# Kernel tuning notes

Hardware: AMD Instinct MI355X
Metric: run time of the kernel (lower is better)

Reference implementation:

```python
import jax, jax.numpy as jnp
import numpy as np

B, C, N, K, H = 8, 64, 4096, 32, 4
D = C // H  # head dim = 16
EPS = 1e-5  # BatchNorm eps (torch default)


def setup_inputs() -> dict:
    key = jax.random.key(0)
    ks = jax.random.split(key, 7)
    s = 0.05
    return {
        "x": jax.random.normal(ks[0], (B, C, N), jnp.float32),
        "wq": jax.random.normal(ks[1], (C, C), jnp.float32) * s,
        "wk": jax.random.normal(ks[2], (C, C), jnp.float32) * s,
        "wv": jax.random.normal(ks[3], (C, C), jnp.float32) * s,
        "w1": jax.random.normal(ks[4], (4 * C, C), jnp.float32) * s,
        "w2": jax.random.normal(ks[5], (C, 4 * C), jnp.float32) * s,
        "g1": jnp.ones((C,), jnp.float32),
        "b1": jnp.zeros((C,), jnp.float32),
        "g2": jnp.ones((C,), jnp.float32),
        "b2": jnp.zeros((C,), jnp.float32),
    }


def _bn(f, g, b):
    # BatchNorm1d in training mode: stats over (batch, points) per channel.
    # f: (B, N, C)
    mu = jnp.mean(f, axis=(0, 1))
    var = jnp.var(f, axis=(0, 1))  # biased, as torch uses for normalization
    return (f - mu) * jax.lax.rsqrt(var + EPS) * g + b


def reference(x, wq, wk, wv, w1, w2, g1, b1, g2, b2):
    feat = jnp.transpose(x, (0, 2, 1))  # (B, N, C)
    # KNN in feature space: negative squared distances, take top-K largest
    sq = jnp.sum(feat * feat, axis=-1)  # (B, N)
    neg_d = 2.0 * jnp.einsum('bnc,bmc->bnm', feat, feat) - sq[:, :, None] - sq[:, None, :]
    _, idx = jax.lax.top_k(neg_d, K)  # (B, N, K) int32
    # gather neighbors and form diffs
    nbrs = jax.vmap(lambda p, i: p[i])(feat, idx)  # (B, N, K, C)
    diff = nbrs - feat[:, :, None, :]
    # 1x1-conv projections (bias-free linear over channels)
    q = jnp.einsum('bnc,oc->bno', feat, wq).reshape(B, N, H, D)
    k = jnp.einsum('bnkc,oc->bnko', diff, wk).reshape(B, N, K, H, D)
    v = jnp.einsum('bnkc,oc->bnko', diff, wv).reshape(B, N, K, H, D)
    energy = jnp.einsum('bnhd,bnkhd->bnhk', q, k) / jnp.sqrt(jnp.float32(D))
    attn = jax.nn.softmax(energy, axis=-1)  # softmax over K neighbors
    out = jnp.einsum('bnhk,bnkhd->bnhd', attn, v).reshape(B, N, C)  # H-major merge
    f1 = _bn(feat + out, g1, b1)
    hid = jnp.einsum('bnc,oc->bno', f1, w1)
    hid = jnp.where(hid > 0, hid, 0.2 * hid)  # LeakyReLU(0.2)
    ff = jnp.einsum('bno,co->bnc', hid, w2)
    f2 = _bn(f1 + ff, g2, b2)
    return jnp.transpose(f2, (0, 2, 1))  # (B, C, N)
```

## Files before the change

### kernel.cpp

```cpp
#include <hip/hip_runtime.h>

#define Bdim 8
#define Cdim 64
#define Ndim 4096
#define Kdim 32
#define ROWS (Bdim*Ndim)
#define BN_EPS 1e-5f

using f32x4  = __attribute__((ext_vector_type(4))) float;
using f16x8  = __attribute__((ext_vector_type(8))) _Float16;

__device__ __forceinline__ float dot4(float4 a, float4 b){
  return a.x*b.x + a.y*b.y + a.z*b.z + a.w*b.w;
}
__device__ __forceinline__ int wofs(int o, int g){ return o*64 + (((g ^ ((o>>2)&7)))<<2); }
__device__ __forceinline__ unsigned keyOf(float f){
  unsigned u = __float_as_uint(f);
  return (u & 0x80000000u) ? ~u : (u ^ 0x80000000u);
}

__global__ __launch_bounds__(256) void prep_proj_kernel(const float* __restrict__ x,
    const float* __restrict__ wq, const float* __restrict__ wk,
    const float* __restrict__ wv,
    float* __restrict__ sq,
    float* __restrict__ Qo, float* __restrict__ PKo, float* __restrict__ PVo,
    float* __restrict__ accZ,
    float* __restrict__ featT, unsigned short* __restrict__ xh)
{
  __shared__ __align__(16) float ftile[64*68];
  __shared__ __align__(16) float Ws[3][64*64];
  const int tid = threadIdx.x;
  const int blk = blockIdx.x;
  const int b  = blk & 7;
  const int n0 = (blk >> 3) * 64;
  const size_t rowBase = (size_t)b*Ndim + n0;
  if (blk == 0) accZ[tid] = 0.f;
  for (int k=0;k<16;++k){
    int idx = tid + (k<<8);
    int c = idx>>6, nn = idx&63;
    ftile[nn*68+c] = x[((size_t)b*64+c)*Ndim + n0 + nn];
  }
  {
    const float* wp[3] = {wq, wk, wv};
    for (int m=0;m<3;++m)
      for (int k=0;k<16;++k){
        int idx = tid + (k<<8);
        int o = idx>>6, c = idx&63;
        Ws[m][wofs(o, c>>2) + (c&3)] = wp[m][o*64 + c];
      }
  }
  __syncthreads();
  for (int k=0;k<16;++k){
    int idx = tid + (k<<8);
    int r = idx>>6, c = idx&63;
    float v = ftile[r*68+c];
    size_t o = (rowBase + r)*64 + c;
    featT[o] = v;
    _Float16 hh = (_Float16)v;
    xh[o] = *reinterpret_cast<unsigned short*>(&hh);
  }
  if (tid < 64){
    float a = 0.f;
    #pragma unroll
    for (int c=0;c<64;++c){ float v = ftile[tid*68+c]; a += v*v; }
    sq[b*Ndim + n0 + tid] = a;
  }
  const int tr = tid>>4, to = tid&15;
  float* outp[3] = {Qo, PKo, PVo};
  for (int m=0;m<3;++m){
    float acc[4][4];
    #pragma unroll
    for (int r=0;r<4;++r){ acc[r][0]=0.f; acc[r][1]=0.f; acc[r][2]=0.f; acc[r][3]=0.f; }
    #pragma unroll 4
    for (int c4=0;c4<16;++c4){
      float4 f[4], w[4];
      #pragma unroll
      for (int r=0;r<4;++r)  f[r] = *(const float4*)&ftile[(4*tr+r)*68 + (c4<<2)];
      #pragma unroll
      for (int oo=0;oo<4;++oo) w[oo] = *(const float4*)&Ws[m][wofs(4*to+oo, c4)];
      #pragma unroll
      for (int r=0;r<4;++r)
        #pragma unroll
        for (int oo=0;oo<4;++oo)
          acc[r][oo] += dot4(f[r], w[oo]);
    }
    #pragma unroll
    for (int r=0;r<4;++r){
      float4 v; v.x=acc[r][0]; v.y=acc[r][1]; v.z=acc[r][2]; v.w=acc[r][3];
      *(float4*)&outp[m][(rowBase + 4*tr + r)*64 + 4*to] = v;
    }
  }
}

__global__ __launch_bounds__(1024) void knn_attn_kernel(
    const float* __restrict__ sq,
    const float* __restrict__ Qm, const float* __restrict__ PKm, const float* __restrict__ PVm,
    const float* __restrict__ featT, const unsigned short* __restrict__ xh,
    float* __restrict__ t1, float* __restrict__ bn1s, float* __restrict__ bn1q)
{
  __shared__ __align__(16) unsigned char smem[43200];
  float* fnS  = (float*)smem;
  float* qvS  = (float*)(smem + 4096);
  float* pknS = (float*)(smem + 8192);
  float* pvnS = (float*)(smem + 12288);
  unsigned short* dbuf = (unsigned short*)(smem + 16384);
  int*   candI  = (int*)(smem + 16384);
  float* red1   = (float*)(smem + 20480);
  float* red2   = (float*)(smem + 24576);
  float* enS    = (float*)(smem + 32896);
  int*   outIdx = (int*)(smem + 41088);
  float* sqnS   = (float*)(smem + 43136);

  const int tid  = threadIdx.x;
  const int lane = tid & 63;
  const int w    = tid >> 6;
  const int blk  = blockIdx.x;
  const int b    = blk & 7;
  const int n0   = (blk >> 3) << 4;
  const size_t b4096 = (size_t)b << 12;

  {
    int j = tid>>6, c = tid&63;
    size_t ro = (b4096 + n0 + j)*64 + c;
    fnS[tid]  = featT[ro];
    qvS[tid]  = Qm[ro];
    pknS[tid] = PKm[ro];
    pvnS[tid] = PVm[ro];
    if (tid < 16) sqnS[tid] = sq[b4096 + n0 + tid];
    if (tid < 512) outIdx[tid] = n0 + (tid>>5);
  }
  __syncthreads();

  const unsigned short* xhb = xh + (b4096 << 6);
  const float* sqb = sq + b4096;
  const int l15  = lane & 15;
  const int acol = (lane >> 4) << 3;
  const int qrow = (lane >> 4) << 2;

  unsigned kk[32];

  {
    f16x8 a0 = *(const f16x8*)&xhb[(size_t)(n0 + l15)*64 + acol];
    f16x8 a1 = *(const f16x8*)&xhb[(size_t)(n0 + l15)*64 + acol + 32];
    #pragma unroll
    for (int ch=0; ch<16; ++ch){
      unsigned short* bw = dbuf + (ch&1)*(16*258);
      const int brow = (ch<<8) + (w<<4) + l15;
      f16x8 b0 = *(const f16x8*)&xhb[(size_t)brow*64 + acol];
      f16x8 b1 = *(const f16x8*)&xhb[(size_t)brow*64 + acol + 32];
      f32x4 acc = {0.f,0.f,0.f,0.f};
      acc = __builtin_amdgcn_mfma_f32_16x16x32_f16(a0, b0, acc, 0, 0, 0);
      acc = __builtin_amdgcn_mfma_f32_16x16x32_f16(a1, b1, acc, 0, 0, 0);
      float sm = sqb[brow];
      #pragma unroll
      for (int r=0;r<4;++r){
        float v = fmaf(2.f, acc[r], -sm);
        int k16 = (int)fmaf(v, 128.f, 40960.f);
        k16 = k16 < 0 ? 0 : (k16 > 65535 ? 65535 : k16);
        bw[(qrow+r)*258 + (w<<4) + l15] = (unsigned short)k16;
      }
      __syncthreads();
      unsigned k01 = *(const unsigned*)&bw[w*258 + (lane<<2)];
      unsigned k23 = *(const unsigned*)&bw[w*258 + (lane<<2) + 2];
      kk[(ch<<1)]   = k01;
      kk[(ch<<1)+1] = k23;
    }
  }

  const unsigned long long below = (1ull<<lane) - 1ull;
  int sQ;
  {
    unsigned mE = 0, mO = 0;
    #pragma unroll
    for (int i=0;i<16;++i){
      unsigned u = kk[i];
      unsigned hv = u >> 16, lv = u & 0xFFFFu;
      unsigned m = hv > lv ? hv : lv;
      mE = mE > m ? mE : m;
    }
    #pragma unroll
    for (int i=16;i<32;++i){
      unsigned u = kk[i];
      unsigned hv = u >> 16, lv = u & 0xFFFFu;
      unsigned m = hv > lv ? hv : lv;
      mO = mO > m ? mO : m;
    }
    unsigned T = 0;
    #pragma unroll
    for (int bit=15; bit>=0; --bit){
      unsigned cand = T | (1u<<bit);
      int c2 = (int)__popcll(__ballot(mE >= cand)) + (int)__popcll(__ballot(mO >= cand));
      if (c2 >= 32) T = cand;
    }
    const unsigned Tm = (T > 16u) ? (T - 16u) : 0u;
    int base = 0;
    #pragma unroll
    for (int j=0;j<64;++j){
      unsigned word = kk[((j>>2)<<1) | ((j>>1)&1)];
      unsigned key  = (j&1) ? (word>>16) : (word & 0xFFFFu);
      bool isc = (key >= Tm);
      unsigned long long mk = __ballot(isc);
      if (isc){
        int slot = base + (int)__popcll(mk & below);
        if (slot < 64) candI[(w<<6)+slot] = ((j>>2)<<8) + (lane<<2) + (j&3);
      }
      base += (int)__popcll(mk);
    }
    if (base > 64){
      base = 0;
      #pragma unroll
      for (int j=0;j<64;++j){
        unsigned word = kk[((j>>2)<<1) | ((j>>1)&1)];
        unsigned key  = (j&1) ? (word>>16) : (word & 0xFFFFu);
        bool isc = (key >= T);
        unsigned long long mk = __ballot(isc);
        if (isc){
          int slot = base + (int)__popcll(mk & below);
          if (slot < 64) candI[(w<<6)+slot] = ((j>>2)<<8) + (lane<<2) + (j&3);
        }
        base += (int)__popcll(mk);
      }
    }
    sQ = base < 64 ? base : 64;
  }

  {
    int mj = -1; unsigned keyE = 0u;
    if (lane < sQ){
      mj = candI[(w<<6)+lane];
      const float* fm = featT + (b4096 + mj)*64;
      const float* fq = fnS + (w<<6);
      float as = 0.f;
      #pragma unroll 4
      for (int d4=0; d4<16; ++d4){
        float4 qv = *(const float4*)&fq[d4<<2];
        float4 mv = *(const float4*)&fm[d4<<2];
        as = fmaf(qv.x, mv.x, as); as = fmaf(qv.y, mv.y, as);
        as = fmaf(qv.z, mv.z, as); as = fmaf(qv.w, mv.w, as);
      }
      float de = (2.f*as - sqnS[w]) - sq[b4096 + mj];
      keyE = keyOf(de);
    }
    unsigned long long C = ((unsigned long long)keyE << 32) |
                           (unsigned long long)(~(unsigned)mj);
    #pragma unroll
    for (int k2=2; k2<=64; k2<<=1){
      #pragma unroll
      for (int j2=k2>>1; j2>=1; j2>>=1){
        unsigned long long P = (unsigned long long)__shfl_xor((long long)C, j2, 64);
        bool lowIdx  = ((lane & j2) == 0);
        bool keepMax = (lowIdx == ((lane & k2) == 0));
        unsigned long long mx = C > P ? C : P;
        unsigned long long mn = C > P ? P : C;
        C = keepMax ? mx : mn;
      }
    }
    if (lane < 32) outIdx[(w<<5)+lane] = (int)(~(unsigned)(C & 0xFFFFFFFFull)) & (Ndim-1);
  }
  __syncthreads();

  #pragma unroll
  for (int p=0;p<2;++p){
    int task = tid + (p<<10);
    int jn = task>>7, h = (task>>5)&3, k2 = task&31;
    int mj = outIdx[(jn<<5)+k2] & (Ndim-1);
    const float4* pk4 = (const float4*)(PKm + (b4096 + mj)*64 + (h<<4));
    const float4* qq4 = (const float4*)&qvS[(jn<<6)+(h<<4)];
    const float4* nn4 = (const float4*)&pknS[(jn<<6)+(h<<4)];
    float e = 0.f;
    #pragma unroll
    for (int d=0;d<4;++d){
      float4 kv = pk4[d], qq = qq4[d], nn = nn4[d];
      e += qq.x*(kv.x-nn.x) + qq.y*(kv.y-nn.y) + qq.z*(kv.z-nn.z) + qq.w*(kv.w-nn.w);
    }
    enS[(jn<<7)+(h<<5)+k2] = e * 0.25f;
  }
  __syncthreads();

  {
    int g = tid>>4, l16 = tid&15;
    int jn = g>>2, h = g&3;
    float* ep = &enS[(jn<<7)+(h<<5)];
    float v0 = ep[l16], v1 = ep[l16+16];
    float mx = fmaxf(v0, v1);
    mx = fmaxf(mx, __shfl_xor(mx, 1, 64));
    mx = fmaxf(mx, __shfl_xor(mx, 2, 64));
    mx = fmaxf(mx, __shfl_xor(mx, 4, 64));
    mx = fmaxf(mx, __shfl_xor(mx, 8, 64));
    v0 = expf(v0-mx); v1 = expf(v1-mx);
    float s = v0+v1;
    s += __shfl_xor(s, 1, 64);
    s += __shfl_xor(s, 2, 64);
    s += __shfl_xor(s, 4, 64);
    s += __shfl_xor(s, 8, 64);
    float inv = 1.f/s;
    ep[l16] = v0*inv; ep[l16+16] = v1*inv;
  }
  __syncthreads();

  float tv;
  {
    int c = lane, h = c>>4;
    float a2 = 0.f;
    #pragma unroll 4
    for (int k2=0;k2<32;++k2){
      int mj = outIdx[(w<<5)+k2] & (Ndim-1);
      a2 += enS[(w<<7)+(h<<5)+k2] * (PVm[(b4096 + mj)*64 + c] - pvnS[(w<<6)+c]);
    }
    tv = fnS[(w<<6)+c] + a2;
    t1[(b4096 + n0 + w)*64 + c] = tv;
  }
  red1[tid] = tv;
  red2[tid] = tv*tv;
  __syncthreads();
  if (tid < 64){
    float S = 0.f, S2 = 0.f;
    #pragma unroll
    for (int j=0;j<16;++j){ S += red1[(j<<6)+tid]; S2 += red2[(j<<6)+tid]; }
    atomicAdd(&bn1s[tid], S);
    atomicAdd(&bn1q[tid], S2);
  }
}

__global__ __launch_bounds__(256) void mlp_kernel(const float* __restrict__ t1,
    const float* __restrict__ w1, const float* __restrict__ w2,
    const float* __restrict__ g1, const float* __restrict__ b1,
    const float* __restrict__ bns, const float* __restrict__ bnq,
    float* __restrict__ t2, float* __restrict__ bn2s, float* __restrict__ bn2q)
{
  __shared__ __align__(16) float f1l[64*68];
  __shared__ __align__(16) float hl[64*68];
  __shared__ __align__(16) float w1s[64*64];
  __shared__ __align__(16) float w2s[64*64];
  __shared__ float mu[64], rs[64], gg[64], bb[64];
  const int tid = threadIdx.x;
  if (tid < 64){
    float m = bns[tid] * (1.f/32768.f);
    float v = bnq[tid] * (1.f/32768.f) - m*m;
    mu[tid] = m; rs[tid] = 1.f/sqrtf(v + BN_EPS);
    gg[tid] = g1[tid]; bb[tid] = b1[tid];
  }
  __syncthreads();
  const size_t rowBase = (size_t)blockIdx.x*64;
  for (int k=0;k<16;++k){
    int idx = tid + (k<<8);
    int r = idx>>6, c = idx&63;
    float v = t1[(rowBase + r)*64 + c];
    f1l[r*68+c] = (v - mu[c])*rs[c]*gg[c] + bb[c];
  }
  const int tr = tid>>4, to = tid&15;
  float ff[4][4];
  #pragma unroll
  for (int r=0;r<4;++r){ ff[r][0]=0.f; ff[r][1]=0.f; ff[r][2]=0.f; ff[r][3]=0.f; }

  for (int hc=0; hc<4; ++hc){
    __syncthreads();
    for (int k=0;k<16;++k){
      int idx = tid + (k<<8);
      int o = idx>>6, c = idx&63;
      w1s[wofs(o, c>>2) + (c&3)] = w1[(size_t)(hc*64+o)*64 + c];
      w2s[wofs(o, c>>2) + (c&3)] = w2[(size_t)o*256 + hc*64 + c];
    }
    __syncthreads();
    float hv[4][4];
    #pragma unroll
    for (int r=0;r<4;++r){ hv[r][0]=0.f; hv[r][1]=0.f; hv[r][2]=0.f; hv[r][3]=0.f; }
    #pragma unroll 4
    for (int c4=0;c4<16;++c4){
      float4 f[4], w[4];
      #pragma unroll
      for (int r=0;r<4;++r)  f[r] = *(const float4*)&f1l[(4*tr+r)*68 + (c4<<2)];
      #pragma unroll
      for (int oo=0;oo<4;++oo) w[oo] = *(const float4*)&w1s[wofs(4*to+oo, c4)];
      #pragma unroll
      for (int r=0;r<4;++r)
        #pragma unroll
        for (int oo=0;oo<4;++oo)
          hv[r][oo] += dot4(f[r], w[oo]);
    }
    #pragma unroll
    for (int r=0;r<4;++r){
      float4 v;
      float x0=hv[r][0], x1=hv[r][1], x2=hv[r][2], x3=hv[r][3];
      v.x = (x0>0.f)?x0:0.2f*x0; v.y = (x1>0.f)?x1:0.2f*x1;
      v.z = (x2>0.f)?x2:0.2f*x2; v.w = (x3>0.f)?x3:0.2f*x3;
      *(float4*)&hl[(4*tr+r)*68 + 4*to] = v;
    }
    __syncthreads();
    #pragma unroll 4
    for (int o4=0;o4<16;++o4){
      float4 h[4], w[4];
      #pragma unroll
      for (int r=0;r<4;++r)  h[r] = *(const float4*)&hl[(4*tr+r)*68 + (o4<<2)];
      #pragma unroll
      for (int oo=0;oo<4;++oo) w[oo] = *(const float4*)&w2s[wofs(4*to+oo, o4)];
      #pragma unroll
      for (int r=0;r<4;++r)
        #pragma unroll
        for (int oo=0;oo<4;++oo)
          ff[r][oo] += dot4(h[r], w[oo]);
    }
  }
  float ls[4]  = {0.f,0.f,0.f,0.f};
  float ls2[4] = {0.f,0.f,0.f,0.f};
  #pragma unroll
  for (int r=0;r<4;++r){
    float4 v;
    v.x = f1l[(4*tr+r)*68 + 4*to+0] + ff[r][0];
    v.y = f1l[(4*tr+r)*68 + 4*to+1] + ff[r][1];
    v.z = f1l[(4*tr+r)*68 + 4*to+2] + ff[r][2];
    v.w = f1l[(4*tr+r)*68 + 4*to+3] + ff[r][3];
    *(float4*)&t2[(rowBase + 4*tr + r)*64 + 4*to] = v;
    ls[0]+=v.x; ls[1]+=v.y; ls[2]+=v.z; ls[3]+=v.w;
    ls2[0]+=v.x*v.x; ls2[1]+=v.y*v.y; ls2[2]+=v.z*v.z; ls2[3]+=v.w*v.w;
  }
  __syncthreads();
  #pragma unroll
  for (int i=0;i<4;++i){
    hl[tr*64 + 4*to + i]        = ls[i];
    hl[1024 + tr*64 + 4*to + i] = ls2[i];
  }
  __syncthreads();
  if (tid < 64){
    float S = 0.f, S2 = 0.f;
    #pragma unroll
    for (int g2=0; g2<16; ++g2){ S += hl[g2*64 + tid]; S2 += hl[1024 + g2*64 + tid]; }
    atomicAdd(&bn2s[tid], S);
    atomicAdd(&bn2q[tid], S2);
  }
}

__global__ __launch_bounds__(256) void final_kernel(const float* __restrict__ t2,
    const float* __restrict__ bns, const float* __restrict__ bnq,
    const float* __restrict__ g2, const float* __restrict__ b2,
    float* __restrict__ out)
{
  __shared__ float tile[64*65];
  __shared__ float mu[64], rs[64], gg[64], bb[64];
  const int tid = threadIdx.x;
  const int b = blockIdx.y;
  const int n0 = blockIdx.x*64;
  if (tid < 64){
    float m = bns[tid] * (1.f/32768.f);
    float v = bnq[tid] * (1.f/32768.f) - m*m;
    mu[tid] = m; rs[tid] = 1.f/sqrtf(v + BN_EPS);
    gg[tid] = g2[tid]; bb[tid] = b2[tid];
  }
  __syncthreads();
  for (int k=0;k<16;++k){
    int idx = tid + (k<<8);
    int r = idx>>6, c = idx&63;
    float v = t2[((size_t)b*Ndim + n0 + r)*64 + c];
    tile[r*65+c] = (v - mu[c])*rs[c]*gg[c] + bb[c];
  }
  __syncthreads();
  for (int k=0;k<16;++k){
    int idx = tid + (k<<8);
    int c = idx>>6, nn = idx&63;
    out[((size_t)b*64 + c)*Ndim + n0 + nn] = tile[nn*65+c];
  }
}

extern "C" void kernel_launch(void* const* d_in, const int* in_sizes, int n_in,
                              void* d_out, int out_size, void* d_ws, size_t ws_size,
                              hipStream_t stream)
{
  (void)in_sizes; (void)n_in; (void)out_size; (void)ws_size;
  const float* x  = (const float*)d_in[0];
  const float* wq = (const float*)d_in[1];
  const float* wk = (const float*)d_in[2];
  const float* wv = (const float*)d_in[3];
  const float* w1 = (const float*)d_in[4];
  const float* w2 = (const float*)d_in[5];
  const float* g1 = (const float*)d_in[6];
  const float* b1 = (const float*)d_in[7];
  const float* g2 = (const float*)d_in[8];
  const float* b2 = (const float*)d_in[9];
  float* out = (float*)d_out;

  const size_t NE = (size_t)ROWS*64;
  float* sq   = (float*)d_ws;
  float* Qb   = sq + ROWS;
  float* PKb  = Qb + NE;
  float* PVb  = PKb + NE;
  float* t1   = PVb + NE;
  float* t2   = t1 + NE;
  float* acc  = t2 + NE;
  unsigned short* xh = (unsigned short*)(acc + 256);

  prep_proj_kernel<<<dim3(512), 256, 0, stream>>>(x, wq, wk, wv, sq, Qb, PKb, PVb, acc, t2, xh);
  knn_attn_kernel<<<dim3(2048), 1024, 0, stream>>>(sq, Qb, PKb, PVb, t2, xh, t1, acc, acc+64);
  mlp_kernel<<<dim3(512), 256, 0, stream>>>(t1, w1, w2, g1, b1, acc, acc+64, t2, acc+128, acc+192);
  final_kernel<<<dim3(64,8), 256, 0, stream>>>(t2, acc+128, acc+192, g2, b2, out);
}
```

Before: 376.6 us.

## Batch KNN distance chunks per barrier and compact candidates with prefix-scan

The distance tile loop now processes two 256-column chunks per __syncthreads, halving the barrier count, and pads LDS rows to 260 shorts. Loading the Q/PK/PV rows is deferred until after the distance phase so their LDS space can be reused for the key buffer. Candidate compaction swaps 64 ballot rounds for a per-lane count plus a wavefront shfl_up prefix scan. The PV gather loop is unrolled further. Shared memory grows to about 47.7 KB, and candidate ordering changes from interleaved to lane-major, which may alter tie handling.

```diff
diff --git a/kernel.cpp b/kernel.cpp
--- a/kernel.cpp
+++ b/kernel.cpp
@@ -98,18 +98,18 @@
     const float* __restrict__ featT, const unsigned short* __restrict__ xh,
     float* __restrict__ t1, float* __restrict__ bn1s, float* __restrict__ bn1q)
 {
-  __shared__ __align__(16) unsigned char smem[43200];
-  float* fnS  = (float*)smem;
-  float* qvS  = (float*)(smem + 4096);
-  float* pknS = (float*)(smem + 8192);
-  float* pvnS = (float*)(smem + 12288);
-  unsigned short* dbuf = (unsigned short*)(smem + 16384);
-  int*   candI  = (int*)(smem + 16384);
-  float* red1   = (float*)(smem + 20480);
-  float* red2   = (float*)(smem + 24576);
-  float* enS    = (float*)(smem + 32896);
-  int*   outIdx = (int*)(smem + 41088);
-  float* sqnS   = (float*)(smem + 43136);
+  __shared__ __align__(16) unsigned char smem[47680];
+  float* fnS   = (float*)smem;
+  unsigned short* dbuf = (unsigned short*)(smem + 4096);
+  float* qvS   = (float*)(smem + 4096);
+  float* pknS  = (float*)(smem + 8192);
+  float* pvnS  = (float*)(smem + 12288);
+  int*   candI = (int*)(smem + 16384);
+  float* enS   = (float*)(smem + 20480);
+  float* red1  = (float*)(smem + 37376);
+  float* red2  = (float*)(smem + 41472);
+  int*   outIdx= (int*)(smem + 45568);
+  float* sqnS  = (float*)(smem + 47616);
 
   const int tid  = threadIdx.x;
   const int lane = tid & 63;
@@ -121,11 +121,7 @@
 
   {
     int j = tid>>6, c = tid&63;
-    size_t ro = (b4096 + n0 + j)*64 + c;
-    fnS[tid]  = featT[ro];
-    qvS[tid]  = Qm[ro];
-    pknS[tid] = PKm[ro];
-    pvnS[tid] = PVm[ro];
+    fnS[tid] = featT[(b4096 + n0 + j)*64 + c];
     if (tid < 16) sqnS[tid] = sq[b4096 + n0 + tid];
     if (tid < 512) outIdx[tid] = n0 + (tid>>5);
   }
@@ -142,32 +138,47 @@
   {
     f16x8 a0 = *(const f16x8*)&xhb[(size_t)(n0 + l15)*64 + acol];
     f16x8 a1 = *(const f16x8*)&xhb[(size_t)(n0 + l15)*64 + acol + 32];
-    #pragma unroll
-    for (int ch=0; ch<16; ++ch){
-      unsigned short* bw = dbuf + (ch&1)*(16*258);
-      const int brow = (ch<<8) + (w<<4) + l15;
-      f16x8 b0 = *(const f16x8*)&xhb[(size_t)brow*64 + acol];
-      f16x8 b1 = *(const f16x8*)&xhb[(size_t)brow*64 + acol + 32];
-      f32x4 acc = {0.f,0.f,0.f,0.f};
-      acc = __builtin_amdgcn_mfma_f32_16x16x32_f16(a0, b0, acc, 0, 0, 0);
-      acc = __builtin_amdgcn_mfma_f32_16x16x32_f16(a1, b1, acc, 0, 0, 0);
-      float sm = sqb[brow];
-      #pragma unroll
-      for (int r=0;r<4;++r){
-        float v = fmaf(2.f, acc[r], -sm);
-        int k16 = (int)fmaf(v, 128.f, 40960.f);
-        k16 = k16 < 0 ? 0 : (k16 > 65535 ? 65535 : k16);
-        bw[(qrow+r)*258 + (w<<4) + l15] = (unsigned short)k16;
+    #pragma unroll 2
+    for (int g=0; g<8; ++g){
+      unsigned short* bw = dbuf + (g&1)*8320;
+      #pragma unroll
+      for (int c2=0;c2<2;++c2){
+        const int ch   = (g<<1) + c2;
+        const int brow = (ch<<8) + (w<<4) + l15;
+        f16x8 b0 = *(const f16x8*)&xhb[(size_t)brow*64 + acol];
+        f16x8 b1 = *(const f16x8*)&xhb[(size_t)brow*64 + acol + 32];
+        f32x4 acc = {0.f,0.f,0.f,0.f};
+        acc = __builtin_amdgcn_mfma_f32_16x16x32_f16(a0, b0, acc, 0, 0, 0);
+        acc = __builtin_amdgcn_mfma_f32_16x16x32_f16(a1, b1, acc, 0, 0, 0);
+        float sm = sqb[brow];
+        #pragma unroll
+        for (int r=0;r<4;++r){
+          float v = fmaf(2.f, acc[r], -sm);
+          int k16 = (int)fmaf(v, 128.f, 40960.f);
+          k16 = k16 < 0 ? 0 : (k16 > 65535 ? 65535 : k16);
+          bw[c2*4160 + (qrow+r)*260 + (w<<4) + l15] = (unsigned short)k16;
+        }
       }
       __syncthreads();
-      unsigned k01 = *(const unsigned*)&bw[w*258 + (lane<<2)];
-      unsigned k23 = *(const unsigned*)&bw[w*258 + (lane<<2) + 2];
-      kk[(ch<<1)]   = k01;
-      kk[(ch<<1)+1] = k23;
-    }
-  }
-
-  const unsigned long long below = (1ull<<lane) - 1ull;
+      #pragma unroll
+      for (int c2=0;c2<2;++c2){
+        const unsigned short* base = bw + c2*4160 + w*260 + (lane<<2);
+        uint2 kp = *(const uint2*)base;
+        kk[((g<<1)+c2)*2]     = kp.x;
+        kk[((g<<1)+c2)*2 + 1] = kp.y;
+      }
+    }
+  }
+  __syncthreads();
+
+  {
+    int j = tid>>6, c = tid&63;
+    size_t ro = (b4096 + n0 + j)*64 + c;
+    qvS[tid]  = Qm[ro];
+    pknS[tid] = PKm[ro];
+    pvnS[tid] = PVm[ro];
+  }
+
   int sQ;
   {
     unsigned mE = 0, mO = 0;
@@ -193,35 +204,37 @@
       if (c2 >= 32) T = cand;
     }
     const unsigned Tm = (T > 16u) ? (T - 16u) : 0u;
-    int base = 0;
-    #pragma unroll
-    for (int j=0;j<64;++j){
-      unsigned word = kk[((j>>2)<<1) | ((j>>1)&1)];
-      unsigned key  = (j&1) ? (word>>16) : (word & 0xFFFFu);
-      bool isc = (key >= Tm);
-      unsigned long long mk = __ballot(isc);
-      if (isc){
-        int slot = base + (int)__popcll(mk & below);
-        if (slot < 64) candI[(w<<6)+slot] = ((j>>2)<<8) + (lane<<2) + (j&3);
-      }
-      base += (int)__popcll(mk);
-    }
-    if (base > 64){
-      base = 0;
-      #pragma unroll
-      for (int j=0;j<64;++j){
-        unsigned word = kk[((j>>2)<<1) | ((j>>1)&1)];
-        unsigned key  = (j&1) ? (word>>16) : (word & 0xFFFFu);
-        bool isc = (key >= T);
-        unsigned long long mk = __ballot(isc);
-        if (isc){
-          int slot = base + (int)__popcll(mk & below);
-          if (slot < 64) candI[(w<<6)+slot] = ((j>>2)<<8) + (lane<<2) + (j&3);
-        }
-        base += (int)__popcll(mk);
-      }
-    }
-    sQ = base < 64 ? base : 64;
+
+    unsigned Tuse = Tm;
+    int lc, ex, tot;
+    while (true){
+      lc = 0;
+      #pragma unroll
+      for (int i=0;i<32;++i){
+        unsigned u = kk[i];
+        lc += ((u & 0xFFFFu) >= Tuse);
+        lc += ((u >> 16)     >= Tuse);
+      }
+      int inc = lc;
+      #pragma unroll
+      for (int off=1; off<64; off<<=1){
+        int nv = __shfl_up(inc, off, 64);
+        if (lane >= off) inc += nv;
+      }
+      ex  = inc - lc;
+      tot = __shfl(inc, 63, 64);
+      if (tot <= 64 || Tuse == T) break;
+      Tuse = T;
+    }
+    int idx = ex;
+    #pragma unroll
+    for (int i=0;i<32;++i){
+      unsigned u = kk[i];
+      int gidx = ((i>>1)<<8) + (lane<<2) + ((i&1)<<1);
+      if ((u & 0xFFFFu) >= Tuse){ if (idx<64) candI[(w<<6)+idx] = gidx;   ++idx; }
+      if ((u >> 16)     >= Tuse){ if (idx<64) candI[(w<<6)+idx] = gidx+1; ++idx; }
+    }
+    sQ = tot < 64 ? tot : 64;
   }
 
   {
@@ -302,7 +315,7 @@
   {
     int c = lane, h = c>>4;
     float a2 = 0.f;
-    #pragma unroll 4
+    #pragma unroll 8
     for (int k2=0;k2<32;++k2){
       int mj = outIdx[(w<<5)+k2] & (Ndim-1);
       a2 += enS[(w<<7)+(h<<5)+k2] * (PVm[(b4096 + mj)*64 + c] - pvnS[(w<<6)+c]);
```

After: 432.6 us. 14.9% more time.
